# Kernel optimization log

Hardware: AMD Instinct MI355X
Metric: run time of the kernel (lower is better)

The kernel has to match this reference:

```python
import jax, jax.numpy as jnp
import numpy as np

NUM_RELS = 19


def rgcn_layer(h, W, b, src, dst, etype, n_nodes):
    """DGL RelGraphConv (basis regularizer, num_bases=num_rels, sum aggregation, bias, no self-loop).

    out[v] = sum_{e: dst(e)=v} W[etype(e)] @ h[src(e)] + b
    Computed as: aggregate h[src] per (relation, dst) pair, then one GEMM per relation.
    """
    # segment id combines relation and destination node -> [R*N] segments
    seg = etype * n_nodes + dst
    agg = jax.ops.segment_sum(h[src], seg, num_segments=NUM_RELS * n_nodes)
    agg = agg.reshape(NUM_RELS, n_nodes, h.shape[1])  # [R, N, in]
    return jnp.einsum('rni,rio->no', agg, W) + b       # [N, out]


def setup_inputs() -> dict:
    key = jax.random.key(0)
    ks = jax.random.split(key, 8)
    N, E, R, D = 100000, 1600000, NUM_RELS, 32
    s = 0.1  # keep activations well-scaled across layers
    return {
        'src': jax.random.randint(ks[0], (E,), 0, N, dtype=jnp.int32),
        'dst': jax.random.randint(ks[1], (E,), 0, N, dtype=jnp.int32),
        'etype': jax.random.randint(ks[2], (E,), 0, R, dtype=jnp.int32),
        'n_nodes': N,
        'W1': jax.random.normal(ks[3], (R, 1, D), jnp.float32) * s,
        'b1': jnp.zeros((D,), jnp.float32),
        'W2': jax.random.normal(ks[4], (R, D, D), jnp.float32) * s,
        'b2': jnp.zeros((D,), jnp.float32),
        'W3': jax.random.normal(ks[5], (D, D), jnp.float32) * s,
        'b3': jnp.zeros((D,), jnp.float32),
    }


def reference(src, dst, etype, n_nodes, W1, b1, W2, b2, W3, b3):
    # h = ones(N, 1), as in Embedder.forward
    h = jnp.ones((n_nodes, 1), jnp.float32)
    h = jax.nn.relu(rgcn_layer(h, W1, b1, src, dst, etype, n_nodes))
    h = jax.nn.relu(rgcn_layer(h, W2, b2, src, dst, etype, n_nodes))
    # conv_output=False -> final layer is a plain Linear
    return h @ W3 + b3
```

## Files before the change

### kernel.cpp

```cpp
#include <hip/hip_runtime.h>

#define NUM_RELS 19
#define NPB 256
#define NPB_SHIFT 8
#define MAXB 400
#define NBLK 512

typedef _Float16 half8 __attribute__((ext_vector_type(8)));
typedef float floatx4 __attribute__((ext_vector_type(4)));


__global__ __launch_bounds__(512) void count_kernel(const int* __restrict__ dst,
                                                    int* __restrict__ blkhist,
                                                    int* __restrict__ bcnt,
                                                    int E, int B, int chunk) {
    __shared__ int h[MAXB];
    for (int i = threadIdx.x; i < B; i += 512) h[i] = 0;
    __syncthreads();
    int e0 = blockIdx.x * chunk, e1 = min(E, e0 + chunk);
    for (int e = e0 + (int)threadIdx.x; e < e1; e += 512)
        atomicAdd(&h[dst[e] >> NPB_SHIFT], 1);
    __syncthreads();
    for (int i = threadIdx.x; i < B; i += 512) {
        blkhist[blockIdx.x * B + i] = h[i];
        if (h[i]) atomicAdd(&bcnt[i], h[i]);
    }
}


__global__ __launch_bounds__(512) void bscan_kernel(const int* __restrict__ bcnt,
                                                    int* __restrict__ pbase, int B) {
    __shared__ int lds[512];
    int t = threadIdx.x;
    int c = (t < B) ? ((bcnt[t] + 7) & ~7) : 0;
    lds[t] = c;
    __syncthreads();
    for (int off = 1; off < 512; off <<= 1) {
        int x = (t >= off) ? lds[t - off] : 0;
        __syncthreads();
        lds[t] += x;
        __syncthreads();
    }
    if (t < B) pbase[t] = lds[t] - c;
}


__global__ __launch_bounds__(NBLK) void offscan_kernel(const int* __restrict__ blkhist,
                                                       const int* __restrict__ pbase,
                                                       int* __restrict__ offs, int B) {
    __shared__ int lds[NBLK];
    int bucket = blockIdx.x;
    int t = threadIdx.x;
    int v = blkhist[t * B + bucket];
    lds[t] = v;
    __syncthreads();
    for (int off = 1; off < NBLK; off <<= 1) {
        int x = (t >= off) ? lds[t - off] : 0;
        __syncthreads();
        lds[t] += x;
        __syncthreads();
    }
    offs[t * B + bucket] = pbase[bucket] + lds[t] - v;
}


__global__ __launch_bounds__(512) void scatter2_kernel(
    const int* __restrict__ src, const int* __restrict__ dst, const int* __restrict__ etype,
    const int* __restrict__ offs, uint2* __restrict__ recs, int E, int B, int chunk) {
    __shared__ int cur[MAXB];
    for (int i = threadIdx.x; i < B; i += 512) cur[i] = offs[blockIdx.x * B + i];
    __syncthreads();
    int e0 = blockIdx.x * chunk, e1 = min(E, e0 + chunk);
    for (int e = e0 + (int)threadIdx.x; e < e1; e += 512) {
        int d = dst[e];
        int b = d >> NPB_SHIFT;
        int pos = atomicAdd(&cur[b], 1);
        uint2 rec;
        rec.x = ((unsigned)src[e] << 5) | (unsigned)etype[e];
        rec.y = (unsigned)d;
        recs[pos] = rec;
    }
}


__global__ __launch_bounds__(256) void bsort_l1_kernel(
    const uint2* __restrict__ recs, const int* __restrict__ pbase, const int* __restrict__ bcnt,
    int* __restrict__ recs2, int* __restrict__ row_start, int* __restrict__ rend,
    const float* __restrict__ W1, const float* __restrict__ b1, float* __restrict__ h1, int N) {
    __shared__ int hist[NPB];
    __shared__ int offsl[NPB];
    __shared__ int cur[NPB];
    __shared__ int cnt2[NPB * NUM_RELS];
    __shared__ float W1s[NUM_RELS * 32];
    __shared__ float b1s[32];
    int b = blockIdx.x;
    int p0 = pbase[b], n = bcnt[b];
    int t = threadIdx.x;

    hist[t] = 0;
    for (int i = t; i < NPB * NUM_RELS; i += 256) cnt2[i] = 0;
    for (int i = t; i < NUM_RELS * 32; i += 256) W1s[i] = W1[i];
    if (t < 32) b1s[t] = b1[t];
    __syncthreads();

    for (int i = t; i < n; i += 256) {
        uint2 rec = recs[p0 + i];
        int ln = rec.y & (NPB - 1);
        atomicAdd(&hist[ln], 1);
        atomicAdd(&cnt2[ln * NUM_RELS + (rec.x & 31)], 1);
    }
    __syncthreads();
    int c = hist[t];
    offsl[t] = c;
    __syncthreads();
    for (int off = 1; off < 256; off <<= 1) {
        int x = (t >= off) ? offsl[t - off] : 0;
        __syncthreads();
        offsl[t] += x;
        __syncthreads();
    }
    int start = p0 + offsl[t] - c;
    cur[t] = start;
    int v = (b << NPB_SHIFT) + t;
    if (v < N) {
        row_start[v] = start;
        rend[v] = start + c;
    }
    __syncthreads();
    for (int i = t; i < n; i += 256) {
        uint2 rec = recs[p0 + i];
        int p = atomicAdd(&cur[rec.y & (NPB - 1)], 1);
        recs2[p] = (int)rec.x;
    }

    int o = t & 31, hw = t >> 5;
    int v0 = b << NPB_SHIFT;
    for (int k = hw; k < NPB; k += 8) {
        int vv = v0 + k;
        if (vv >= N) break;
        float acc = b1s[o];
        const int* cp = &cnt2[k * NUM_RELS];
#pragma unroll
        for (int r = 0; r < NUM_RELS; ++r) acc += (float)cp[r] * W1s[r * 32 + o];
        h1[(size_t)vv * 32 + o] = fmaxf(acc, 0.f);
    }
}


__global__ void w2swz_kernel(const float* __restrict__ W2, _Float16* __restrict__ W2F) {
    int idx = blockIdx.x * blockDim.x + threadIdx.x;
    if (idx >= NUM_RELS * 2 * 64 * 8) return;
    int j = idx & 7, lane = (idx >> 3) & 63, nt = (idx >> 9) & 1, r = idx >> 10;
    int k = (lane >> 4) * 8 + j, n = nt * 16 + (lane & 15);
    W2F[idx] = (_Float16)W2[r * 1024 + k * 32 + n];
}


__global__ __launch_bounds__(256) void transform_kernel(
    const float* __restrict__ h1, const _Float16* __restrict__ W2F,
    _Float16* __restrict__ g, int N) {
    int lane = threadIdx.x & 63;
    int tile = blockIdx.x * 4 + (threadIdx.x >> 6);
    int v0 = tile * 16;
    if (v0 >= N) return;

    const float* hrow = h1 + (size_t)(v0 + (lane & 15)) * 32 + (lane >> 4) * 8;
    float4 p0 = *(const float4*)hrow;
    float4 p1 = *(const float4*)(hrow + 4);
    half8 a;
    a[0] = (_Float16)p0.x; a[1] = (_Float16)p0.y; a[2] = (_Float16)p0.z; a[3] = (_Float16)p0.w;
    a[4] = (_Float16)p1.x; a[5] = (_Float16)p1.y; a[6] = (_Float16)p1.z; a[7] = (_Float16)p1.w;

    floatx4 zero = {0.f, 0.f, 0.f, 0.f};
    int row = (lane >> 4) * 4;
    int col = lane & 15;
    for (int r = 0; r < NUM_RELS; ++r) {
        _Float16* gbase = g + ((size_t)r * N + v0) * 32;
#pragma unroll
        for (int nt = 0; nt < 2; ++nt) {
            half8 bfrag = *(const half8*)(W2F + ((r * 2 + nt) * 64 + lane) * 8);
            floatx4 d = __builtin_amdgcn_mfma_f32_16x16x32_f16(a, bfrag, zero, 0, 0, 0);
#pragma unroll
            for (int reg = 0; reg < 4; ++reg) {
                gbase[(row + reg) * 32 + nt * 16 + col] = (_Float16)d[reg];
            }
        }
    }
}


__global__ __launch_bounds__(1024) void edge23_kernel(
    const _Float16* __restrict__ g, const int* __restrict__ row_start,
    const int* __restrict__ rend, const int* __restrict__ recs2,
    const float* __restrict__ b2, const float* __restrict__ W3, const float* __restrict__ b3,
    float* __restrict__ out, int N) {
    __shared__ float W3s[1024];
    __shared__ float b2s[32], b3s[32];
    W3s[threadIdx.x] = W3[threadIdx.x];
    if (threadIdx.x < 32) {
        b2s[threadIdx.x] = b2[threadIdx.x];
        b3s[threadIdx.x] = b3[threadIdx.x];
    }
    __syncthreads();

    int o = threadIdx.x & 31;
    int hw = blockIdx.x * 32 + (threadIdx.x >> 5);
    if (hw >= N) return;
    int start = row_start[hw], end = rend[hw];
    const int sN32 = N * 32;

    float acc = b2s[o];
    for (int base = start; base < end; base += 32) {
        int idx = base + o;
        int m_l = (idx < end) ? recs2[idx] : 0;
        int cnt = min(32, end - base);
        int j = 0;
        for (; j + 8 <= cnt; j += 8) {
            float x[8];
#pragma unroll
            for (int k = 0; k < 8; ++k) {
                int m = __shfl(m_l, j + k, 32);
                x[k] = (float)g[(m & 31) * sN32 + (m >> 5) * 32 + o];
            }
            acc += (((x[0] + x[1]) + (x[2] + x[3])) + ((x[4] + x[5]) + (x[6] + x[7])));
        }
        for (; j + 4 <= cnt; j += 4) {
            float x[4];
#pragma unroll
            for (int k = 0; k < 4; ++k) {
                int m = __shfl(m_l, j + k, 32);
                x[k] = (float)g[(m & 31) * sN32 + (m >> 5) * 32 + o];
            }
            acc += ((x[0] + x[1]) + (x[2] + x[3]));
        }
        for (; j < cnt; ++j) {
            int m = __shfl(m_l, j, 32);
            acc += (float)g[(m & 31) * sN32 + (m >> 5) * 32 + o];
        }
    }
    float h2v = fmaxf(acc, 0.f);

    float acc3 = b3s[o];
#pragma unroll
    for (int i = 0; i < 32; ++i) {
        float hi = __shfl(h2v, i, 32);
        acc3 = fmaf(hi, W3s[i * 32 + o], acc3);
    }
    out[(size_t)hw * 32 + o] = acc3;
}


extern "C" void kernel_launch(void* const* d_in, const int* in_sizes, int n_in,
                              void* d_out, int out_size, void* d_ws, size_t ws_size,
                              hipStream_t stream) {
    const int* src   = (const int*)d_in[0];
    const int* dst   = (const int*)d_in[1];
    const int* etype = (const int*)d_in[2];
    const float* W1  = (const float*)d_in[4];
    const float* b1  = (const float*)d_in[5];
    const float* W2  = (const float*)d_in[6];
    const float* b2  = (const float*)d_in[7];
    const float* W3  = (const float*)d_in[8];
    const float* b3  = (const float*)d_in[9];
    float* out = (float*)d_out;

    int E = in_sizes[0];
    int N = out_size / 32;
    int B = (N + NPB - 1) >> NPB_SHIFT;

    char* ws = (char*)d_ws;
    size_t off = 0;
    auto alloc = [&](size_t bytes) {
        void* p = ws + off;
        off = (off + bytes + 255) & ~(size_t)255;
        return p;
    };
    float* h1      = (float*)alloc((size_t)N * 32 * 4);
    int* bcnt      = (int*)alloc((size_t)MAXB * 4);
    int* pbase     = (int*)alloc((size_t)MAXB * 4);
    int* blkhist   = (int*)alloc((size_t)NBLK * MAXB * 4);
    int* offs      = (int*)alloc((size_t)NBLK * MAXB * 4);
    int* row_start = (int*)alloc((size_t)N * 4);
    int* rend      = (int*)alloc((size_t)N * 4);
    uint2* recs    = (uint2*)alloc(((size_t)E + 8 * MAXB + 64) * 8);
    int* recs2     = (int*)alloc(((size_t)E + 8 * MAXB + 64) * 4);
    _Float16* g    = (_Float16*)alloc((size_t)NUM_RELS * N * 32 * 2);
    _Float16* W2F  = (_Float16*)alloc((size_t)NUM_RELS * 2 * 64 * 8 * 2);

    hipMemsetAsync(bcnt, 0, (size_t)B * 4, stream);

    int chunk = (E + NBLK - 1) / NBLK;
    count_kernel<<<NBLK, 512, 0, stream>>>(dst, blkhist, bcnt, E, B, chunk);
    bscan_kernel<<<1, 512, 0, stream>>>(bcnt, pbase, B);
    offscan_kernel<<<B, NBLK, 0, stream>>>(blkhist, pbase, offs, B);
    scatter2_kernel<<<NBLK, 512, 0, stream>>>(src, dst, etype, offs, recs, E, B, chunk);

    bsort_l1_kernel<<<B, 256, 0, stream>>>(recs, pbase, bcnt, recs2, row_start, rend,
                                           W1, b1, h1, N);

    w2swz_kernel<<<(NUM_RELS * 2 * 64 * 8 + 255) / 256, 256, 0, stream>>>(W2, W2F);
    int ntiles = (N + 15) / 16;
    transform_kernel<<<(ntiles + 3) / 4, 256, 0, stream>>>(h1, W2F, g, N);

    edge23_kernel<<<(N + 31) / 32, 1024, 0, stream>>>(g, row_start, rend, recs2, b2, W3, b3, out, N);
}
```

Baseline: 240.7 us.

## Pack sort records to 32 bits, fuse scans, store h1 in fp16, shrink edge blocks

Edge records are packed into one 32-bit word (local dst in the high bits, src and etype below) instead of a uint2, which halves scatter and bucket-sort traffic. The pbase scan is folded into offscan so every block recomputes it, the bcnt memset is folded into the W2 swizzle kernel, and two launches go away. h1 is stored as fp16 so transform reads it directly. The edge kernel drops to 512-thread blocks and loses the 8-wide unrolled gather. Risks are redundant scan work across blocks and less memory-level parallelism in the gather.

```diff
diff --git a/kernel.cpp b/kernel.cpp
--- a/kernel.cpp
+++ b/kernel.cpp
@@ -8,6 +8,18 @@
 
 typedef _Float16 half8 __attribute__((ext_vector_type(8)));
 typedef float floatx4 __attribute__((ext_vector_type(4)));
+
+
+
+__global__ void w2swz_kernel(const float* __restrict__ W2, _Float16* __restrict__ W2F,
+                             int* __restrict__ bcnt, int B) {
+    int idx = blockIdx.x * blockDim.x + threadIdx.x;
+    if (idx < B) bcnt[idx] = 0;
+    if (idx >= NUM_RELS * 2 * 64 * 8) return;
+    int j = idx & 7, lane = (idx >> 3) & 63, nt = (idx >> 9) & 1, r = idx >> 10;
+    int k = (lane >> 4) * 8 + j, n = nt * 16 + (lane & 15);
+    W2F[idx] = (_Float16)W2[r * 1024 + k * 32 + n];
+}
 
 
 __global__ __launch_bounds__(512) void count_kernel(const int* __restrict__ dst,
@@ -28,29 +40,31 @@
 }
 
 
-__global__ __launch_bounds__(512) void bscan_kernel(const int* __restrict__ bcnt,
-                                                    int* __restrict__ pbase, int B) {
-    __shared__ int lds[512];
+__global__ __launch_bounds__(NBLK) void offscan_kernel(const int* __restrict__ blkhist,
+                                                       const int* __restrict__ bcnt,
+                                                       int* __restrict__ pbase,
+                                                       int* __restrict__ offs, int B) {
+    __shared__ int lds[NBLK];
+    __shared__ int pbs;
+    int bucket = blockIdx.x;
     int t = threadIdx.x;
+
     int c = (t < B) ? ((bcnt[t] + 7) & ~7) : 0;
     lds[t] = c;
     __syncthreads();
-    for (int off = 1; off < 512; off <<= 1) {
+    for (int off = 1; off < NBLK; off <<= 1) {
         int x = (t >= off) ? lds[t - off] : 0;
         __syncthreads();
         lds[t] += x;
         __syncthreads();
     }
-    if (t < B) pbase[t] = lds[t] - c;
-}
-
-
-__global__ __launch_bounds__(NBLK) void offscan_kernel(const int* __restrict__ blkhist,
-                                                       const int* __restrict__ pbase,
-                                                       int* __restrict__ offs, int B) {
-    __shared__ int lds[NBLK];
-    int bucket = blockIdx.x;
-    int t = threadIdx.x;
+    if (t == bucket) {
+        pbs = lds[t] - c;
+        pbase[bucket] = pbs;
+    }
+    __syncthreads();
+    int myp = pbs;
+
     int v = blkhist[t * B + bucket];
     lds[t] = v;
     __syncthreads();
@@ -60,13 +74,13 @@
         lds[t] += x;
         __syncthreads();
     }
-    offs[t * B + bucket] = pbase[bucket] + lds[t] - v;
+    offs[t * B + bucket] = myp + lds[t] - v;
 }
 
 
 __global__ __launch_bounds__(512) void scatter2_kernel(
     const int* __restrict__ src, const int* __restrict__ dst, const int* __restrict__ etype,
-    const int* __restrict__ offs, uint2* __restrict__ recs, int E, int B, int chunk) {
+    const int* __restrict__ offs, unsigned* __restrict__ recs4, int E, int B, int chunk) {
     __shared__ int cur[MAXB];
     for (int i = threadIdx.x; i < B; i += 512) cur[i] = offs[blockIdx.x * B + i];
     __syncthreads();
@@ -75,18 +89,15 @@
         int d = dst[e];
         int b = d >> NPB_SHIFT;
         int pos = atomicAdd(&cur[b], 1);
-        uint2 rec;
-        rec.x = ((unsigned)src[e] << 5) | (unsigned)etype[e];
-        rec.y = (unsigned)d;
-        recs[pos] = rec;
+        recs4[pos] = ((unsigned)(d & (NPB - 1)) << 22) | ((unsigned)src[e] << 5) | (unsigned)etype[e];
     }
 }
 
 
 __global__ __launch_bounds__(256) void bsort_l1_kernel(
-    const uint2* __restrict__ recs, const int* __restrict__ pbase, const int* __restrict__ bcnt,
+    const unsigned* __restrict__ recs4, const int* __restrict__ pbase, const int* __restrict__ bcnt,
     int* __restrict__ recs2, int* __restrict__ row_start, int* __restrict__ rend,
-    const float* __restrict__ W1, const float* __restrict__ b1, float* __restrict__ h1, int N) {
+    const float* __restrict__ W1, const float* __restrict__ b1, _Float16* __restrict__ h1, int N) {
     __shared__ int hist[NPB];
     __shared__ int offsl[NPB];
     __shared__ int cur[NPB];
@@ -104,10 +115,10 @@
     __syncthreads();
 
     for (int i = t; i < n; i += 256) {
-        uint2 rec = recs[p0 + i];
-        int ln = rec.y & (NPB - 1);
+        unsigned rec = recs4[p0 + i];
+        int ln = rec >> 22;
         atomicAdd(&hist[ln], 1);
-        atomicAdd(&cnt2[ln * NUM_RELS + (rec.x & 31)], 1);
+        atomicAdd(&cnt2[ln * NUM_RELS + (rec & 31)], 1);
     }
     __syncthreads();
     int c = hist[t];
@@ -128,9 +139,9 @@
     }
     __syncthreads();
     for (int i = t; i < n; i += 256) {
-        uint2 rec = recs[p0 + i];
-        int p = atomicAdd(&cur[rec.y & (NPB - 1)], 1);
-        recs2[p] = (int)rec.x;
+        unsigned rec = recs4[p0 + i];
+        int p = atomicAdd(&cur[rec >> 22], 1);
+        recs2[p] = (int)(rec & 0x3FFFFFu);
     }
 
     int o = t & 31, hw = t >> 5;
@@ -142,34 +153,20 @@
         const int* cp = &cnt2[k * NUM_RELS];
 #pragma unroll
         for (int r = 0; r < NUM_RELS; ++r) acc += (float)cp[r] * W1s[r * 32 + o];
-        h1[(size_t)vv * 32 + o] = fmaxf(acc, 0.f);
-    }
-}
-
-
-__global__ void w2swz_kernel(const float* __restrict__ W2, _Float16* __restrict__ W2F) {
-    int idx = blockIdx.x * blockDim.x + threadIdx.x;
-    if (idx >= NUM_RELS * 2 * 64 * 8) return;
-    int j = idx & 7, lane = (idx >> 3) & 63, nt = (idx >> 9) & 1, r = idx >> 10;
-    int k = (lane >> 4) * 8 + j, n = nt * 16 + (lane & 15);
-    W2F[idx] = (_Float16)W2[r * 1024 + k * 32 + n];
+        h1[(size_t)vv * 32 + o] = (_Float16)fmaxf(acc, 0.f);
+    }
 }
 
 
 __global__ __launch_bounds__(256) void transform_kernel(
-    const float* __restrict__ h1, const _Float16* __restrict__ W2F,
+    const _Float16* __restrict__ h1, const _Float16* __restrict__ W2F,
     _Float16* __restrict__ g, int N) {
     int lane = threadIdx.x & 63;
     int tile = blockIdx.x * 4 + (threadIdx.x >> 6);
     int v0 = tile * 16;
     if (v0 >= N) return;
 
-    const float* hrow = h1 + (size_t)(v0 + (lane & 15)) * 32 + (lane >> 4) * 8;
-    float4 p0 = *(const float4*)hrow;
-    float4 p1 = *(const float4*)(hrow + 4);
-    half8 a;
-    a[0] = (_Float16)p0.x; a[1] = (_Float16)p0.y; a[2] = (_Float16)p0.z; a[3] = (_Float16)p0.w;
-    a[4] = (_Float16)p1.x; a[5] = (_Float16)p1.y; a[6] = (_Float16)p1.z; a[7] = (_Float16)p1.w;
+    half8 a = *(const half8*)(h1 + (size_t)(v0 + (lane & 15)) * 32 + (lane >> 4) * 8);
 
     floatx4 zero = {0.f, 0.f, 0.f, 0.f};
     int row = (lane >> 4) * 4;
@@ -189,14 +186,14 @@
 }
 
 
-__global__ __launch_bounds__(1024) void edge23_kernel(
+__global__ __launch_bounds__(512) void edge23_kernel(
     const _Float16* __restrict__ g, const int* __restrict__ row_start,
     const int* __restrict__ rend, const int* __restrict__ recs2,
     const float* __restrict__ b2, const float* __restrict__ W3, const float* __restrict__ b3,
     float* __restrict__ out, int N) {
     __shared__ float W3s[1024];
     __shared__ float b2s[32], b3s[32];
-    W3s[threadIdx.x] = W3[threadIdx.x];
+    for (int i = threadIdx.x; i < 1024; i += 512) W3s[i] = W3[i];
     if (threadIdx.x < 32) {
         b2s[threadIdx.x] = b2[threadIdx.x];
         b3s[threadIdx.x] = b3[threadIdx.x];
@@ -204,7 +201,7 @@
     __syncthreads();
 
     int o = threadIdx.x & 31;
-    int hw = blockIdx.x * 32 + (threadIdx.x >> 5);
+    int hw = blockIdx.x * 16 + (threadIdx.x >> 5);
     if (hw >= N) return;
     int start = row_start[hw], end = rend[hw];
     const int sN32 = N * 32;
@@ -215,15 +212,6 @@
         int m_l = (idx < end) ? recs2[idx] : 0;
         int cnt = min(32, end - base);
         int j = 0;
-        for (; j + 8 <= cnt; j += 8) {
-            float x[8];
-#pragma unroll
-            for (int k = 0; k < 8; ++k) {
-                int m = __shfl(m_l, j + k, 32);
-                x[k] = (float)g[(m & 31) * sN32 + (m >> 5) * 32 + o];
-            }
-            acc += (((x[0] + x[1]) + (x[2] + x[3])) + ((x[4] + x[5]) + (x[6] + x[7])));
-        }
         for (; j + 4 <= cnt; j += 4) {
             float x[4];
 #pragma unroll
@@ -275,32 +263,30 @@
         off = (off + bytes + 255) & ~(size_t)255;
         return p;
     };
-    float* h1      = (float*)alloc((size_t)N * 32 * 4);
-    int* bcnt      = (int*)alloc((size_t)MAXB * 4);
-    int* pbase     = (int*)alloc((size_t)MAXB * 4);
-    int* blkhist   = (int*)alloc((size_t)NBLK * MAXB * 4);
-    int* offs      = (int*)alloc((size_t)NBLK * MAXB * 4);
-    int* row_start = (int*)alloc((size_t)N * 4);
-    int* rend      = (int*)alloc((size_t)N * 4);
-    uint2* recs    = (uint2*)alloc(((size_t)E + 8 * MAXB + 64) * 8);
-    int* recs2     = (int*)alloc(((size_t)E + 8 * MAXB + 64) * 4);
-    _Float16* g    = (_Float16*)alloc((size_t)NUM_RELS * N * 32 * 2);
-    _Float16* W2F  = (_Float16*)alloc((size_t)NUM_RELS * 2 * 64 * 8 * 2);
-
-    hipMemsetAsync(bcnt, 0, (size_t)B * 4, stream);
+    _Float16* h1    = (_Float16*)alloc((size_t)N * 32 * 2);
+    int* bcnt       = (int*)alloc((size_t)MAXB * 4);
+    int* pbase      = (int*)alloc((size_t)MAXB * 4);
+    int* blkhist    = (int*)alloc((size_t)NBLK * MAXB * 4);
+    int* offs       = (int*)alloc((size_t)NBLK * MAXB * 4);
+    int* row_start  = (int*)alloc((size_t)N * 4);
+    int* rend       = (int*)alloc((size_t)N * 4);
+    unsigned* recs4 = (unsigned*)alloc(((size_t)E + 8 * MAXB + 64) * 4);
+    int* recs2      = (int*)alloc(((size_t)E + 8 * MAXB + 64) * 4);
+    _Float16* g     = (_Float16*)alloc((size_t)NUM_RELS * N * 32 * 2);
+    _Float16* W2F   = (_Float16*)alloc((size_t)NUM_RELS * 2 * 64 * 8 * 2);
+
+    w2swz_kernel<<<(NUM_RELS * 2 * 64 * 8 + 255) / 256, 256, 0, stream>>>(W2, W2F, bcnt, B);
 
     int chunk = (E + NBLK - 1) / NBLK;
     count_kernel<<<NBLK, 512, 0, stream>>>(dst, blkhist, bcnt, E, B, chunk);
-    bscan_kernel<<<1, 512, 0, stream>>>(bcnt, pbase, B);
-    offscan_kernel<<<B, NBLK, 0, stream>>>(blkhist, pbase, offs, B);
-    scatter2_kernel<<<NBLK, 512, 0, stream>>>(src, dst, etype, offs, recs, E, B, chunk);
-
-    bsort_l1_kernel<<<B, 256, 0, stream>>>(recs, pbase, bcnt, recs2, row_start, rend,
+    offscan_kernel<<<B, NBLK, 0, stream>>>(blkhist, bcnt, pbase, offs, B);
+    scatter2_kernel<<<NBLK, 512, 0, stream>>>(src, dst, etype, offs, recs4, E, B, chunk);
+
+    bsort_l1_kernel<<<B, 256, 0, stream>>>(recs4, pbase, bcnt, recs2, row_start, rend,
                                            W1, b1, h1, N);
 
-    w2swz_kernel<<<(NUM_RELS * 2 * 64 * 8 + 255) / 256, 256, 0, stream>>>(W2, W2F);
     int ntiles = (N + 15) / 16;
     transform_kernel<<<(ntiles + 3) / 4, 256, 0, stream>>>(h1, W2F, g, N);
 
-    edge23_kernel<<<(N + 31) / 32, 1024, 0, stream>>>(g, row_start, rend, recs2, b2, W3, b3, out, N);
-}
+    edge23_kernel<<<(N + 15) / 16, 512, 0, stream>>>(g, row_start, rend, recs2, b2, W3, b3, out, N);
+}
```

After: 230.8 us. -4.1%, faster.
